# Kernel optimization log

Hardware: AMD Instinct MI355X
Metric: run time of the kernel (lower is better)

Reference implementation:

```python
import jax, jax.numpy as jnp
import numpy as np

N = 40000    # nodes
E = 400000   # edges
H = 128      # hidden_channels
G = 50       # num_gaussians
L = 3        # num_interactions
NG = 256     # number of graphs in the batch
CUTOFF = 6.0


def setup_inputs() -> dict:
    key = jax.random.key(0)
    ks = jax.random.split(key, 16)

    def w(k, shape, fan_in):
        return (jax.random.normal(k, shape, jnp.float32) / np.float32(np.sqrt(fan_in)))

    inp = {}
    inp["atomic_numbers"] = jax.random.randint(ks[0], (N,), 0, 100)
    inp["pos"] = jax.random.normal(ks[1], (N, 3), jnp.float32) * 5.0
    inp["edge_index"] = jax.random.randint(ks[2], (2, E), 0, N)
    inp["batch_ids"] = jnp.sort(jax.random.randint(ks[3], (N,), 0, NG))
    inp["embed"] = w(ks[4], (100, H), 1.0)
    inp["msg_w1"] = w(ks[5], (L, H, H), H)
    inp["msg_b1"] = jnp.zeros((L, H), jnp.float32)
    inp["msg_w2"] = w(ks[6], (L, H, 3 * H), H)
    inp["msg_b2"] = jnp.zeros((L, 3 * H), jnp.float32)
    inp["filt_w"] = w(ks[7], (L, G, 3 * H), G)
    inp["filt_b"] = jnp.zeros((L, 3 * H), jnp.float32)
    inp["vec_w"] = w(ks[8], (L, H, 2 * H), H)
    inp["upd_w1"] = w(ks[9], (L, 2 * H, H), 2 * H)
    inp["upd_b1"] = jnp.zeros((L, H), jnp.float32)
    inp["upd_w2"] = w(ks[10], (L, H, 3 * H), H)
    inp["upd_b2"] = jnp.zeros((L, 3 * H), jnp.float32)
    inp["ro_w1"] = w(ks[11], (H, H // 2), H)
    inp["ro_b1"] = jnp.zeros((H // 2,), jnp.float32)
    inp["ro_w2"] = w(ks[12], (H // 2, 1), H // 2)
    inp["ro_b2"] = jnp.zeros((1,), jnp.float32)
    return inp


def _painn(atomic_numbers, pos, edge_index, batch_ids, embed,
           msg_w1, msg_b1, msg_w2, msg_b2, filt_w, filt_b, vec_w,
           upd_w1, upd_b1, upd_w2, upd_b2, ro_w1, ro_b1, ro_w2, ro_b2):
    src, dst = edge_index[0], edge_index[1]
    n = atomic_numbers.shape[0]

    # geometry
    dvec = pos[src] - pos[dst]                              # [E,3]
    dist = jnp.linalg.norm(dvec, axis=-1)                   # [E]
    dvec_n = dvec / (dist[:, None] + 1e-8)                  # [E,3]

    # Gaussian smearing (RBF expansion of distances)
    offset = jnp.linspace(0.0, CUTOFF, G).astype(jnp.float32)
    coeff = -0.5 / (offset[1] - offset[0]) ** 2
    rbf = jnp.exp(coeff * (dist[:, None] - offset[None, :]) ** 2)  # [E,G]

    s = embed[atomic_numbers]                               # [N,H]
    v = jnp.zeros((n, 3, H), s.dtype)                       # [N,3,H]

    for i in range(L):
        # --- message block ---
        w = rbf @ filt_w[i] + filt_b[i]                     # [E,3H]
        s_all = jax.nn.relu(s @ msg_w1[i] + msg_b1[i]) @ msg_w2[i] + msg_b2[i]  # [N,3H]
        gate = s_all[src] * w                               # [E,3H]
        g0, g1, g2 = jnp.split(gate, 3, axis=-1)            # each [E,H]
        ds_e = g0
        dv_e = v[src] * g1[:, None, :] + dvec_n[:, :, None] * g2[:, None, :]  # [E,3,H]
        ds = jax.ops.segment_sum(ds_e, dst, num_segments=n)
        dv = jax.ops.segment_sum(dv_e, dst, num_segments=n)
        s = s + ds
        v = v + dv

        # --- update block ---
        vt = v @ vec_w[i]                                   # [N,3,2H]
        V1, V2 = jnp.split(vt, 2, axis=-1)                  # [N,3,H] each
        v_norm = jnp.linalg.norm(V1, axis=1)                # [N,H]
        u = (jax.nn.relu(jnp.concatenate([s, v_norm], axis=-1) @ upd_w1[i] + upd_b1[i])
             @ upd_w2[i] + upd_b2[i])                       # [N,3H]
        a, b, c = jnp.split(u, 3, axis=-1)
        s = s + a
        v = v * b[:, None, :] + V2 * c[:, None, :]

    # readout + global mean pool
    y = jax.nn.relu(s @ ro_w1 + ro_b1) @ ro_w2 + ro_b2      # [N,1]
    summed = jax.ops.segment_sum(y, batch_ids, num_segments=NG)
    counts = jax.ops.segment_sum(jnp.ones((n, 1), y.dtype), batch_ids, num_segments=NG)
    return summed / jnp.maximum(counts, 1.0)                # [NG,1]


def reference(atomic_numbers, pos, edge_index, batch_ids, embed,
              msg_w1, msg_b1, msg_w2, msg_b2, filt_w, filt_b, vec_w,
              upd_w1, upd_b1, upd_w2, upd_b2, ro_w1, ro_b1, ro_w2, ro_b2):
    return _painn(atomic_numbers, pos, edge_index, batch_ids, embed,
                  msg_w1, msg_b1, msg_w2, msg_b2, filt_w, filt_b, vec_w,
                  upd_w1, upd_b1, upd_w2, upd_b2, ro_w1, ro_b1, ro_w2, ro_b2)
```

## Files before the change

kernel.cpp:

```cpp
#include <hip/hip_runtime.h>
#include <hip/hip_bf16.h>
#include <math.h>


#define N_NODES 40000
#define N_EDGES 400000
#define NGAUSS  50
#define NLAY    3
#define NGRAPH  256

#define WS_BYTES (448ull * 1024 * 1024)
__device__ __align__(256) unsigned char g_ws[WS_BYTES];

typedef __attribute__((ext_vector_type(8))) short short8;
typedef __attribute__((ext_vector_type(4))) float f32x4;

__device__ __forceinline__ float relu_f(float x) { return fmaxf(x, 0.f); }
__device__ __forceinline__ unsigned short f2b(float x) {
  __hip_bfloat16 h = __float2bfloat16(x);
  return *reinterpret_cast<unsigned short*>(&h);
}
__device__ __forceinline__ float b2f(unsigned short u) {
  return __uint_as_float(((unsigned int)u) << 16);
}
__device__ __forceinline__ float b2f_lo(unsigned int u) {
  return __uint_as_float(u << 16);
}
__device__ __forceinline__ float b2f_hi(unsigned int u) {
  return __uint_as_float(u & 0xffff0000u);
}

__global__ __launch_bounds__(256) void cvt_kernel(const float* __restrict__ in,
                                                  unsigned short* __restrict__ out,
                                                  int n) {
  int i = blockIdx.x * 256 + threadIdx.x;
  if (i < n) out[i] = f2b(in[i]);
}

__global__ __launch_bounds__(256) void geom_kernel(const int* __restrict__ src,
                                                   const int* __restrict__ dst,
                                                   const float* __restrict__ pos,
                                                   float4* __restrict__ geom) {
  int e = blockIdx.x * 256 + threadIdx.x;
  if (e >= N_EDGES) return;
  int s = src[e], d = dst[e];
  float dx = pos[s * 3 + 0] - pos[d * 3 + 0];
  float dy = pos[s * 3 + 1] - pos[d * 3 + 1];
  float dz = pos[s * 3 + 2] - pos[d * 3 + 2];
  float dist = sqrtf(dx * dx + dy * dy + dz * dz);
  float inv = 1.f / (dist + 1e-8f);
  geom[e] = make_float4(dx * inv, dy * inv, dz * inv, dist);
}

__global__ __launch_bounds__(256) void hist_kernel(const int* __restrict__ dst,
                                                   int* __restrict__ deg) {
  int e = blockIdx.x * 256 + threadIdx.x;
  if (e < N_EDGES) atomicAdd(&deg[dst[e]], 1);
}

__global__ __launch_bounds__(1024) void scan_kernel(const int* __restrict__ deg,
                                                    int* __restrict__ off, int n) {
  __shared__ int wsum[16];
  __shared__ int ctot;
  int t = threadIdx.x, lane = t & 63, w = t >> 6;
  int carry = 0;
  for (int base = 0; base < n; base += 1024) {
    int i = base + t;
    int v = (i < n) ? deg[i] : 0;
    int x = v;
#pragma unroll
    for (int dd = 1; dd < 64; dd <<= 1) {
      int y = __shfl_up(x, dd);
      if (lane >= dd) x += y;
    }
    if (lane == 63) wsum[w] = x;
    __syncthreads();
    if (w == 0 && lane < 16) {
      int self = wsum[lane];
      int xs = self;
#pragma unroll
      for (int dd = 1; dd < 16; dd <<= 1) {
        int y = __shfl_up(xs, dd);
        if (lane >= dd) xs += y;
      }
      wsum[lane] = xs - self;
      if (lane == 15) ctot = xs;
    }
    __syncthreads();
    if (i < n) off[i] = carry + wsum[w] + (x - v);
    carry += ctot;
    __syncthreads();
  }
  if (t == 0) off[n] = carry;
}

__global__ __launch_bounds__(256) void fill_kernel(const int* __restrict__ dst,
                                                   const int* __restrict__ off,
                                                   int* __restrict__ cursor,
                                                   int* __restrict__ eid) {
  int e = blockIdx.x * 256 + threadIdx.x;
  if (e >= N_EDGES) return;
  int d = dst[e];
  int p = atomicAdd(&cursor[d], 1);
  eid[off[d] + p] = e;
}

__global__ __launch_bounds__(256) void init_kernel(const int* __restrict__ z,
                                                   const float* __restrict__ embed,
                                                   float* __restrict__ s,
                                                   unsigned short* __restrict__ sb,
                                                   unsigned short* __restrict__ vb) {
  int idx = blockIdx.x * 256 + threadIdx.x;
  if (idx < N_NODES * 384) vb[idx] = 0;
  if (idx < N_NODES * 128) {
    int node = idx >> 7, c = idx & 127;
    float val = embed[z[node] * 128 + c];
    s[idx] = val;
    sb[idx] = f2b(val);
  }
}

#define KMAX 256
__global__ __launch_bounds__(256) void gemm_bf16(
    const unsigned short* __restrict__ A1, int lda1,
    const unsigned short* __restrict__ A2, int lda2, int kSplit,
    const unsigned short* __restrict__ B, int ldb,
    const float* __restrict__ bias,
    void* __restrict__ C, int ldc, int M, int K, int doRelu, int outBf16) {
  __shared__ unsigned int Bt32[64][KMAX / 2 + 4];
  int t = threadIdx.x;
  int lane = t & 63, w = t >> 6;
  int n0 = blockIdx.x * 64, m0 = blockIdx.y * 128;
  {
    int c4 = (t & 15) * 4;
    for (int k = (t >> 4) * 2; k < K; k += 32) {
      uint2 va = *(const uint2*)&B[(size_t)k * ldb + n0 + c4];
      uint2 vb = *(const uint2*)&B[(size_t)(k + 1) * ldb + n0 + c4];
      Bt32[c4 + 0][k >> 1] = (va.x & 0xffffu) | (vb.x << 16);
      Bt32[c4 + 1][k >> 1] = (va.x >> 16) | (vb.x & 0xffff0000u);
      Bt32[c4 + 2][k >> 1] = (va.y & 0xffffu) | (vb.y << 16);
      Bt32[c4 + 3][k >> 1] = (va.y >> 16) | (vb.y & 0xffff0000u);
    }
  }
  __syncthreads();

  int row = lane & 15;
  int kg = lane >> 4;

  f32x4 acc[2][4];
#pragma unroll
  for (int rf = 0; rf < 2; ++rf)
#pragma unroll
    for (int nf = 0; nf < 4; ++nf) acc[rf][nf] = (f32x4){0.f, 0.f, 0.f, 0.f};

  for (int ks = 0; ks < K; ks += 32) {
    int kk = ks + kg * 8;
    short8 af[2];
#pragma unroll
    for (int rf = 0; rf < 2; ++rf) {
      int mrow = m0 + w * 32 + rf * 16 + row;
      if (mrow >= M) mrow = M - 1;
      const unsigned short* Ap;
      int kloc;
      if (kk < kSplit) { Ap = A1 + (size_t)mrow * lda1; kloc = kk; }
      else             { Ap = A2 + (size_t)mrow * lda2; kloc = kk - kSplit; }
      af[rf] = *(const short8*)&Ap[kloc];
    }
#pragma unroll
    for (int nf = 0; nf < 4; ++nf) {
      short8 bf = *(const short8*)((const unsigned short*)Bt32[nf * 16 + row] + kk);
#pragma unroll
      for (int rf = 0; rf < 2; ++rf)
        acc[rf][nf] = __builtin_amdgcn_mfma_f32_16x16x32_bf16(af[rf], bf,
                                                              acc[rf][nf], 0, 0, 0);
    }
  }

#pragma unroll
  for (int rf = 0; rf < 2; ++rf)
#pragma unroll
    for (int nf = 0; nf < 4; ++nf)
#pragma unroll
      for (int r = 0; r < 4; ++r) {
        int gr = m0 + w * 32 + rf * 16 + kg * 4 + r;
        int gc = n0 + nf * 16 + row;
        if (gr < M) {
          float val = acc[rf][nf][r] + (bias ? bias[gc] : 0.f);
          if (doRelu) val = relu_f(val);
          if (outBf16) ((unsigned short*)C)[(size_t)gr * ldc + gc] = f2b(val);
          else         ((float*)C)[(size_t)gr * ldc + gc] = val;
        }
      }
}

__global__ __launch_bounds__(256) void msg_kernel(const int* __restrict__ off,
                                                  const int* __restrict__ eid_arr,
                                                  const int* __restrict__ src_arr,
                                                  const float4* __restrict__ geom,
                                                  const unsigned short* __restrict__ s_all_b,
                                                  const unsigned short* __restrict__ fwb,
                                                  const float* __restrict__ fb,
                                                  const float* __restrict__ s_in,
                                                  const unsigned short* __restrict__ v_in_b,
                                                  float* __restrict__ s_out,
                                                  unsigned short* __restrict__ s_out_b,
                                                  unsigned short* __restrict__ v_out_b) {
  int node = blockIdx.x * 4 + (threadIdx.x >> 6);
  if (node >= N_NODES) return;
  int lane = threadIdx.x & 63;
  int c2 = lane * 2;
  const float DELTA = 6.0f / 49.0f;
  const float INVD = 49.0f / 6.0f;
  const float CO = -0.5f * INVD * INVD;
  float fbr[3][2];
#pragma unroll
  for (int jj = 0; jj < 3; ++jj) {
    float2 f = *(const float2*)&fb[jj * 128 + c2];
    fbr[jj][0] = f.x; fbr[jj][1] = f.y;
  }
  float ds[2] = {0.f, 0.f};
  float dv[3][2] = {{0.f}};
  int e0 = off[node], e1 = off[node + 1];

  for (int q = e0; q < e1; ++q) {
    int e = eid_arr[q];
    int s = src_arr[e];
    float4 gm = geom[e];
    float d = gm.w;
    float wv[3][2];
#pragma unroll
    for (int jj = 0; jj < 3; ++jj) { wv[jj][0] = fbr[jj][0]; wv[jj][1] = fbr[jj][1]; }
    int glo = max(0, (int)ceilf(d * INVD - 8.f));
    int ghi = min(NGAUSS - 1, (int)floorf(d * INVD + 8.f));
    for (int g = glo; g <= ghi; ++g) {
      float diff = d - g * DELTA;
      float r = __expf(CO * diff * diff);
      const unsigned short* fr = fwb + (size_t)g * 384 + c2;
#pragma unroll
      for (int jj = 0; jj < 3; ++jj) {
        unsigned int f = *(const unsigned int*)&fr[jj * 128];
        wv[jj][0] = fmaf(r, b2f_lo(f), wv[jj][0]);
        wv[jj][1] = fmaf(r, b2f_hi(f), wv[jj][1]);
      }
    }
    const unsigned short* pas = s_all_b + (size_t)s * 384 + c2;
    const unsigned short* pav = v_in_b + (size_t)s * 384 + c2;
    unsigned int a_s[3] = {*(const unsigned int*)&pas[0],
                           *(const unsigned int*)&pas[128],
                           *(const unsigned int*)&pas[256]};
    unsigned int a_v[3] = {*(const unsigned int*)&pav[0],
                           *(const unsigned int*)&pav[128],
                           *(const unsigned int*)&pav[256]};
    float gt[3][2];
#pragma unroll
    for (int jj = 0; jj < 3; ++jj) {
      gt[jj][0] = b2f_lo(a_s[jj]) * wv[jj][0];
      gt[jj][1] = b2f_hi(a_s[jj]) * wv[jj][1];
    }
    ds[0] += gt[0][0];
    ds[1] += gt[0][1];
    float dn[3] = {gm.x, gm.y, gm.z};
#pragma unroll
    for (int dd = 0; dd < 3; ++dd) {
      dv[dd][0] = fmaf(b2f_lo(a_v[dd]), gt[1][0], fmaf(dn[dd], gt[2][0], dv[dd][0]));
      dv[dd][1] = fmaf(b2f_hi(a_v[dd]), gt[1][1], fmaf(dn[dd], gt[2][1], dv[dd][1]));
    }
  }

  size_t sb = (size_t)node * 128 + c2;
  float2 si = *(const float2*)&s_in[sb];
  float2 so = make_float2(si.x + ds[0], si.y + ds[1]);
  *(float2*)&s_out[sb] = so;
  *(unsigned int*)&s_out_b[sb] =
      (unsigned int)f2b(so.x) | ((unsigned int)f2b(so.y) << 16);
#pragma unroll
  for (int dd = 0; dd < 3; ++dd) {
    size_t vb = (size_t)node * 384 + dd * 128 + c2;
    unsigned int vi = *(const unsigned int*)&v_in_b[vb];
    float vo0 = b2f_lo(vi) + dv[dd][0];
    float vo1 = b2f_hi(vi) + dv[dd][1];
    *(unsigned int*)&v_out_b[vb] =
        (unsigned int)f2b(vo0) | ((unsigned int)f2b(vo1) << 16);
  }
}

__global__ __launch_bounds__(256) void vnorm_kernel(const unsigned short* __restrict__ V12b,
                                                    unsigned short* __restrict__ vnb) {
  int idx = blockIdx.x * 256 + threadIdx.x;
  if (idx >= N_NODES * 32) return;
  int node = idx >> 5, c4 = (idx & 31) * 4;
  size_t b = (size_t)node * 768 + c4;
  ushort4 x = *(const ushort4*)&V12b[b];
  ushort4 y = *(const ushort4*)&V12b[b + 256];
  ushort4 zz = *(const ushort4*)&V12b[b + 512];
  ushort4 o;
  o.x = f2b(sqrtf(b2f(x.x) * b2f(x.x) + b2f(y.x) * b2f(y.x) + b2f(zz.x) * b2f(zz.x)));
  o.y = f2b(sqrtf(b2f(x.y) * b2f(x.y) + b2f(y.y) * b2f(y.y) + b2f(zz.y) * b2f(zz.y)));
  o.z = f2b(sqrtf(b2f(x.z) * b2f(x.z) + b2f(y.z) * b2f(y.z) + b2f(zz.z) * b2f(zz.z)));
  o.w = f2b(sqrtf(b2f(x.w) * b2f(x.w) + b2f(y.w) * b2f(y.w) + b2f(zz.w) * b2f(zz.w)));
  *(ushort4*)&vnb[(size_t)node * 128 + c4] = o;
}

__global__ __launch_bounds__(256) void update_kernel(const float* __restrict__ s_msg,
                                                     const unsigned short* __restrict__ v_msg_b,
                                                     const unsigned short* __restrict__ u_b,
                                                     const unsigned short* __restrict__ V12b,
                                                     float* __restrict__ s_out,
                                                     unsigned short* __restrict__ s_out_b,
                                                     unsigned short* __restrict__ v_out_b) {
  int idx = blockIdx.x * 256 + threadIdx.x;
  if (idx >= N_NODES * 32) return;
  int node = idx >> 5, c4 = (idx & 31) * 4;
  size_t ub = (size_t)node * 384 + c4;
  ushort4 a4 = *(const ushort4*)&u_b[ub];
  ushort4 b4 = *(const ushort4*)&u_b[ub + 128];
  ushort4 c4v = *(const ushort4*)&u_b[ub + 256];
  size_t sb = (size_t)node * 128 + c4;
  float4 sm = *(const float4*)&s_msg[sb];
  float4 so = make_float4(sm.x + b2f(a4.x), sm.y + b2f(a4.y),
                          sm.z + b2f(a4.z), sm.w + b2f(a4.w));
  *(float4*)&s_out[sb] = so;
  ushort4 sob = {f2b(so.x), f2b(so.y), f2b(so.z), f2b(so.w)};
  *(ushort4*)&s_out_b[sb] = sob;
  float bb[4] = {b2f(b4.x), b2f(b4.y), b2f(b4.z), b2f(b4.w)};
  float cc[4] = {b2f(c4v.x), b2f(c4v.y), b2f(c4v.z), b2f(c4v.w)};
#pragma unroll
  for (int dd = 0; dd < 3; ++dd) {
    size_t vb = (size_t)node * 384 + dd * 128 + c4;
    size_t vbv = (size_t)node * 768 + dd * 256 + 128 + c4;
    ushort4 vm = *(const ushort4*)&v_msg_b[vb];
    ushort4 v2 = *(const ushort4*)&V12b[vbv];
    ushort4 vo;
    vo.x = f2b(b2f(vm.x) * bb[0] + b2f(v2.x) * cc[0]);
    vo.y = f2b(b2f(vm.y) * bb[1] + b2f(v2.y) * cc[1]);
    vo.z = f2b(b2f(vm.z) * bb[2] + b2f(v2.z) * cc[2]);
    vo.w = f2b(b2f(vm.w) * bb[3] + b2f(v2.w) * cc[3]);
    *(ushort4*)&v_out_b[vb] = vo;
  }
}

__global__ __launch_bounds__(256) void readout2_kernel(const float* __restrict__ ro_h,
                                                       const float* __restrict__ w2,
                                                       const int* __restrict__ batch,
                                                       float* __restrict__ pool,
                                                       float* __restrict__ cnt) {
  int node = blockIdx.x * 4 + (threadIdx.x >> 6);
  if (node >= N_NODES) return;
  int lane = threadIdx.x & 63;
  float y = ro_h[(size_t)node * 64 + lane] * w2[lane];
#pragma unroll
  for (int o = 32; o > 0; o >>= 1) y += __shfl_xor(y, o);
  if (lane == 0) {
    int b = batch[node];
    atomicAdd(&pool[b], y);
    atomicAdd(&cnt[b], 1.0f);
  }
}

__global__ void final_kernel(const float* __restrict__ pool,
                             const float* __restrict__ cnt,
                             const float* __restrict__ b2,
                             float* __restrict__ out) {
  int g = threadIdx.x;
  if (g < NGRAPH) out[g] = (pool[g] + cnt[g] * b2[0]) / fmaxf(cnt[g], 1.0f);
}

extern "C" void kernel_launch(void* const* d_in, const int* in_sizes, int n_in,
                              void* d_out, int out_size, void* d_ws, size_t ws_size,
                              hipStream_t stream) {
  const int*   z      = (const int*)d_in[0];
  const float* pos    = (const float*)d_in[1];
  const int*   esrc   = (const int*)d_in[2];
  const int*   edst   = esrc + N_EDGES;
  const int*   batch  = (const int*)d_in[3];
  const float* embed  = (const float*)d_in[4];
  const float* msg_w1 = (const float*)d_in[5];
  const float* msg_b1 = (const float*)d_in[6];
  const float* msg_w2 = (const float*)d_in[7];
  const float* msg_b2 = (const float*)d_in[8];
  const float* filt_w = (const float*)d_in[9];
  const float* filt_b = (const float*)d_in[10];
  const float* vec_w  = (const float*)d_in[11];
  const float* upd_w1 = (const float*)d_in[12];
  const float* upd_b1 = (const float*)d_in[13];
  const float* upd_w2 = (const float*)d_in[14];
  const float* upd_b2 = (const float*)d_in[15];
  const float* ro_w1  = (const float*)d_in[16];
  const float* ro_b1  = (const float*)d_in[17];
  const float* ro_w2  = (const float*)d_in[18];
  const float* ro_b2  = (const float*)d_in[19];
  (void)in_sizes; (void)n_in; (void)out_size;

  void* wsp = nullptr;
  if (hipGetSymbolAddress(&wsp, HIP_SYMBOL(g_ws)) != hipSuccess || wsp == nullptr) {
    wsp = d_ws;
  }
  char* wsb = (char*)wsp;
  size_t o = 0;
  auto alloc = [&](size_t bytes) -> void* {
    void* p = wsb + o;
    o += (bytes + 255) & ~(size_t)255;
    return p;
  };
  float4* geom   = (float4*)alloc(sizeof(float4) * N_EDGES);
  int* csr_off   = (int*)alloc(4ull * (N_NODES + 1));
  int* deg       = (int*)alloc(4ull * N_NODES);
  int* cursor    = (int*)alloc(4ull * N_NODES);
  int* csr_eid   = (int*)alloc(4ull * N_EDGES);
  float* sA      = (float*)alloc(4ull * N_NODES * 128);
  float* sB      = (float*)alloc(4ull * N_NODES * 128);
  float* ro_h    = (float*)alloc(4ull * N_NODES * 64);
  unsigned short* s_all_b = (unsigned short*)alloc(2ull * N_NODES * 384);
  unsigned short* sAb    = (unsigned short*)alloc(2ull * N_NODES * 128);
  unsigned short* sBb    = (unsigned short*)alloc(2ull * N_NODES * 128);
  unsigned short* vAb    = (unsigned short*)alloc(2ull * N_NODES * 384);
  unsigned short* vBb    = (unsigned short*)alloc(2ull * N_NODES * 384);
  unsigned short* vnb    = (unsigned short*)alloc(2ull * N_NODES * 128);
  unsigned short* hidden = (unsigned short*)alloc(2ull * N_NODES * 128);
  unsigned short* Vbuf_b = (unsigned short*)alloc(2ull * N_NODES * 768);
  unsigned short* ubuf_b = (unsigned short*)alloc(2ull * N_NODES * 384);
  unsigned short* wb_m1  = (unsigned short*)alloc(2ull * NLAY * 128 * 128);
  unsigned short* wb_m2  = (unsigned short*)alloc(2ull * NLAY * 128 * 384);
  unsigned short* wb_vw  = (unsigned short*)alloc(2ull * NLAY * 128 * 256);
  unsigned short* wb_u1  = (unsigned short*)alloc(2ull * NLAY * 256 * 128);
  unsigned short* wb_u2  = (unsigned short*)alloc(2ull * NLAY * 128 * 384);
  unsigned short* wb_fw  = (unsigned short*)alloc(2ull * NLAY * 50 * 384);
  unsigned short* wb_ro  = (unsigned short*)alloc(2ull * 128 * 64);
  float* pool    = (float*)alloc(4ull * NGRAPH);
  float* cnt     = (float*)alloc(4ull * NGRAPH);

  if (wsb == (char*)d_ws && o > ws_size) return;

  hipMemsetAsync(deg, 0, 4ull * N_NODES, stream);
  hipMemsetAsync(cursor, 0, 4ull * N_NODES, stream);
  hipMemsetAsync(pool, 0, 4ull * NGRAPH, stream);
  hipMemsetAsync(cnt, 0, 4ull * NGRAPH, stream);

  auto cvt = [&](const float* in, unsigned short* out, int n) {
    cvt_kernel<<<(n + 255) / 256, 256, 0, stream>>>(in, out, n);
  };
  cvt(msg_w1, wb_m1, NLAY * 128 * 128);
  cvt(msg_w2, wb_m2, NLAY * 128 * 384);
  cvt(vec_w,  wb_vw, NLAY * 128 * 256);
  cvt(upd_w1, wb_u1, NLAY * 256 * 128);
  cvt(upd_w2, wb_u2, NLAY * 128 * 384);
  cvt(filt_w, wb_fw, NLAY * 50 * 384);
  cvt(ro_w1,  wb_ro, 128 * 64);

  geom_kernel<<<(N_EDGES + 255) / 256, 256, 0, stream>>>(esrc, edst, pos, geom);
  hist_kernel<<<(N_EDGES + 255) / 256, 256, 0, stream>>>(edst, deg);
  scan_kernel<<<1, 1024, 0, stream>>>(deg, csr_off, N_NODES);
  fill_kernel<<<(N_EDGES + 255) / 256, 256, 0, stream>>>(edst, csr_off, cursor, csr_eid);
  init_kernel<<<(N_NODES * 384 + 255) / 256, 256, 0, stream>>>(z, embed, sA, sAb, vAb);

  const int BIG = 1 << 30;
  const int GY40 = (N_NODES + 127) / 128;
  const int GY120 = (N_NODES * 3 + 127) / 128;
  for (int i = 0; i < NLAY; ++i) {
    const float* mb1 = msg_b1 + (size_t)i * 128;
    const float* mb2 = msg_b2 + (size_t)i * 384;
    const float* fbv = filt_b + (size_t)i * 384;
    const float* ub1 = upd_b1 + (size_t)i * 128;
    const float* ub2 = upd_b2 + (size_t)i * 384;
    const unsigned short* m1 = wb_m1 + (size_t)i * 128 * 128;
    const unsigned short* m2 = wb_m2 + (size_t)i * 128 * 384;
    const unsigned short* vw = wb_vw + (size_t)i * 128 * 256;
    const unsigned short* u1 = wb_u1 + (size_t)i * 256 * 128;
    const unsigned short* u2 = wb_u2 + (size_t)i * 128 * 384;
    const unsigned short* fwb = wb_fw + (size_t)i * 50 * 384;

    gemm_bf16<<<dim3(2, GY40), 256, 0, stream>>>(sAb, 128, sAb, 128, BIG, m1, 128, mb1,
                                                 hidden, 128, N_NODES, 128, 1, 1);
    gemm_bf16<<<dim3(6, GY40), 256, 0, stream>>>(hidden, 128, hidden, 128, BIG, m2, 384,
                                                 mb2, s_all_b, 384, N_NODES, 128, 0, 1);
    msg_kernel<<<N_NODES / 4, 256, 0, stream>>>(csr_off, csr_eid, esrc, geom,
                                                s_all_b, fwb, fbv, sA, vAb,
                                                sB, sBb, vBb);
    gemm_bf16<<<dim3(4, GY120), 256, 0, stream>>>(vBb, 128, vBb, 128, BIG, vw, 256,
                                                  nullptr, Vbuf_b, 256, N_NODES * 3,
                                                  128, 0, 1);
    vnorm_kernel<<<(N_NODES * 32 + 255) / 256, 256, 0, stream>>>(Vbuf_b, vnb);
    gemm_bf16<<<dim3(2, GY40), 256, 0, stream>>>(sBb, 128, vnb, 128, 128, u1, 128, ub1,
                                                 hidden, 128, N_NODES, 256, 1, 1);
    gemm_bf16<<<dim3(6, GY40), 256, 0, stream>>>(hidden, 128, hidden, 128, BIG, u2, 384,
                                                 ub2, ubuf_b, 384, N_NODES, 128, 0, 1);
    update_kernel<<<(N_NODES * 32 + 255) / 256, 256, 0, stream>>>(sB, vBb, ubuf_b,
                                                                  Vbuf_b, sA, sAb, vAb);
  }

  gemm_bf16<<<dim3(1, GY40), 256, 0, stream>>>(sAb, 128, sAb, 128, BIG, wb_ro, 64,
                                               ro_b1, ro_h, 64, N_NODES, 128, 1, 0);
  readout2_kernel<<<N_NODES / 4, 256, 0, stream>>>(ro_h, ro_w2, batch, pool, cnt);
  final_kernel<<<1, 256, 0, stream>>>(pool, cnt, ro_b2, (float*)d_out);
}
```

Measured before the change: 1.253 ms.

## Keep A tile in registers and loop over all N columns per block

Result: slower. 1.443 ms (+15.2%).

```diff
diff --git a/kernel.cpp b/kernel.cpp
--- a/kernel.cpp
+++ b/kernel.cpp
@@ -120,77 +120,88 @@
   }
 }
 
-#define KMAX 256
+template <int K>
 __global__ __launch_bounds__(256) void gemm_bf16(
     const unsigned short* __restrict__ A1, int lda1,
     const unsigned short* __restrict__ A2, int lda2, int kSplit,
     const unsigned short* __restrict__ B, int ldb,
     const float* __restrict__ bias,
-    void* __restrict__ C, int ldc, int M, int K, int doRelu, int outBf16) {
-  __shared__ unsigned int Bt32[64][KMAX / 2 + 4];
+    void* __restrict__ C, int ldc, int M, int N, int doRelu, int outBf16) {
+  constexpr int KS = K / 32;
+  __shared__ unsigned int Bt32[64][K / 2 + 4];
   int t = threadIdx.x;
   int lane = t & 63, w = t >> 6;
-  int n0 = blockIdx.x * 64, m0 = blockIdx.y * 128;
-  {
-    int c4 = (t & 15) * 4;
-    for (int k = (t >> 4) * 2; k < K; k += 32) {
-      uint2 va = *(const uint2*)&B[(size_t)k * ldb + n0 + c4];
-      uint2 vb = *(const uint2*)&B[(size_t)(k + 1) * ldb + n0 + c4];
-      Bt32[c4 + 0][k >> 1] = (va.x & 0xffffu) | (vb.x << 16);
-      Bt32[c4 + 1][k >> 1] = (va.x >> 16) | (vb.x & 0xffff0000u);
-      Bt32[c4 + 2][k >> 1] = (va.y & 0xffffu) | (vb.y << 16);
-      Bt32[c4 + 3][k >> 1] = (va.y >> 16) | (vb.y & 0xffff0000u);
-    }
-  }
-  __syncthreads();
-
+  int m0 = blockIdx.x * 128;
   int row = lane & 15;
   int kg = lane >> 4;
 
-  f32x4 acc[2][4];
-#pragma unroll
-  for (int rf = 0; rf < 2; ++rf)
-#pragma unroll
-    for (int nf = 0; nf < 4; ++nf) acc[rf][nf] = (f32x4){0.f, 0.f, 0.f, 0.f};
-
-  for (int ks = 0; ks < K; ks += 32) {
-    int kk = ks + kg * 8;
-    short8 af[2];
-#pragma unroll
-    for (int rf = 0; rf < 2; ++rf) {
-      int mrow = m0 + w * 32 + rf * 16 + row;
-      if (mrow >= M) mrow = M - 1;
+  short8 af[2][KS];
+#pragma unroll
+  for (int rf = 0; rf < 2; ++rf) {
+    int mrow = m0 + w * 32 + rf * 16 + row;
+    if (mrow >= M) mrow = M - 1;
+#pragma unroll
+    for (int ks = 0; ks < KS; ++ks) {
+      int kk = ks * 32 + kg * 8;
       const unsigned short* Ap;
       int kloc;
       if (kk < kSplit) { Ap = A1 + (size_t)mrow * lda1; kloc = kk; }
       else             { Ap = A2 + (size_t)mrow * lda2; kloc = kk - kSplit; }
-      af[rf] = *(const short8*)&Ap[kloc];
-    }
-#pragma unroll
-    for (int nf = 0; nf < 4; ++nf) {
-      short8 bf = *(const short8*)((const unsigned short*)Bt32[nf * 16 + row] + kk);
-#pragma unroll
-      for (int rf = 0; rf < 2; ++rf)
-        acc[rf][nf] = __builtin_amdgcn_mfma_f32_16x16x32_bf16(af[rf], bf,
-                                                              acc[rf][nf], 0, 0, 0);
-    }
-  }
-
-#pragma unroll
-  for (int rf = 0; rf < 2; ++rf)
-#pragma unroll
-    for (int nf = 0; nf < 4; ++nf)
-#pragma unroll
-      for (int r = 0; r < 4; ++r) {
-        int gr = m0 + w * 32 + rf * 16 + kg * 4 + r;
-        int gc = n0 + nf * 16 + row;
-        if (gr < M) {
-          float val = acc[rf][nf][r] + (bias ? bias[gc] : 0.f);
-          if (doRelu) val = relu_f(val);
-          if (outBf16) ((unsigned short*)C)[(size_t)gr * ldc + gc] = f2b(val);
-          else         ((float*)C)[(size_t)gr * ldc + gc] = val;
+      af[rf][ks] = *(const short8*)&Ap[kloc];
+    }
+  }
+
+  for (int n0 = 0; n0 < N; n0 += 64) {
+    {
+      int c4 = (t & 15) * 4;
+#pragma unroll
+      for (int k = (t >> 4) * 2; k < K; k += 32) {
+        uint2 va = *(const uint2*)&B[(size_t)k * ldb + n0 + c4];
+        uint2 vb = *(const uint2*)&B[(size_t)(k + 1) * ldb + n0 + c4];
+        Bt32[c4 + 0][k >> 1] = (va.x & 0xffffu) | (vb.x << 16);
+        Bt32[c4 + 1][k >> 1] = (va.x >> 16) | (vb.x & 0xffff0000u);
+        Bt32[c4 + 2][k >> 1] = (va.y & 0xffffu) | (vb.y << 16);
+        Bt32[c4 + 3][k >> 1] = (va.y >> 16) | (vb.y & 0xffff0000u);
+      }
+    }
+    __syncthreads();
+
+    f32x4 acc[2][4];
+#pragma unroll
+    for (int rf = 0; rf < 2; ++rf)
+#pragma unroll
+      for (int nf = 0; nf < 4; ++nf) acc[rf][nf] = (f32x4){0.f, 0.f, 0.f, 0.f};
+
+#pragma unroll
+    for (int ks = 0; ks < KS; ++ks) {
+      int kk = ks * 32 + kg * 8;
+#pragma unroll
+      for (int nf = 0; nf < 4; ++nf) {
+        short8 bf = *(const short8*)((const unsigned short*)Bt32[nf * 16 + row] + kk);
+#pragma unroll
+        for (int rf = 0; rf < 2; ++rf)
+          acc[rf][nf] = __builtin_amdgcn_mfma_f32_16x16x32_bf16(af[rf][ks], bf,
+                                                                acc[rf][nf], 0, 0, 0);
+      }
+    }
+
+#pragma unroll
+    for (int rf = 0; rf < 2; ++rf)
+#pragma unroll
+      for (int nf = 0; nf < 4; ++nf)
+#pragma unroll
+        for (int r = 0; r < 4; ++r) {
+          int gr = m0 + w * 32 + rf * 16 + kg * 4 + r;
+          int gc = n0 + nf * 16 + row;
+          if (gr < M) {
+            float val = acc[rf][nf][r] + (bias ? bias[gc] : 0.f);
+            if (doRelu) val = relu_f(val);
+            if (outBf16) ((unsigned short*)C)[(size_t)gr * ldc + gc] = f2b(val);
+            else         ((float*)C)[(size_t)gr * ldc + gc] = val;
+          }
         }
-      }
+    __syncthreads();
+  }
 }
 
 __global__ __launch_bounds__(256) void msg_kernel(const int* __restrict__ off,
@@ -469,27 +480,27 @@
     const unsigned short* u2 = wb_u2 + (size_t)i * 128 * 384;
     const unsigned short* fwb = wb_fw + (size_t)i * 50 * 384;
 
-    gemm_bf16<<<dim3(2, GY40), 256, 0, stream>>>(sAb, 128, sAb, 128, BIG, m1, 128, mb1,
-                                                 hidden, 128, N_NODES, 128, 1, 1);
-    gemm_bf16<<<dim3(6, GY40), 256, 0, stream>>>(hidden, 128, hidden, 128, BIG, m2, 384,
-                                                 mb2, s_all_b, 384, N_NODES, 128, 0, 1);
+    gemm_bf16<128><<<GY40, 256, 0, stream>>>(sAb, 128, sAb, 128, BIG, m1, 128, mb1,
+                                             hidden, 128, N_NODES, 128, 1, 1);
+    gemm_bf16<128><<<GY40, 256, 0, stream>>>(hidden, 128, hidden, 128, BIG, m2, 384,
+                                             mb2, s_all_b, 384, N_NODES, 384, 0, 1);
     msg_kernel<<<N_NODES / 4, 256, 0, stream>>>(csr_off, csr_eid, esrc, geom,
                                                 s_all_b, fwb, fbv, sA, vAb,
                                                 sB, sBb, vBb);
-    gemm_bf16<<<dim3(4, GY120), 256, 0, stream>>>(vBb, 128, vBb, 128, BIG, vw, 256,
-                                                  nullptr, Vbuf_b, 256, N_NODES * 3,
-                                                  128, 0, 1);
+    gemm_bf16<128><<<GY120, 256, 0, stream>>>(vBb, 128, vBb, 128, BIG, vw, 256,
+                                              nullptr, Vbuf_b, 256, N_NODES * 3, 256,
+                                              0, 1);
     vnorm_kernel<<<(N_NODES * 32 + 255) / 256, 256, 0, stream>>>(Vbuf_b, vnb);
-    gemm_bf16<<<dim3(2, GY40), 256, 0, stream>>>(sBb, 128, vnb, 128, 128, u1, 128, ub1,
-                                                 hidden, 128, N_NODES, 256, 1, 1);
-    gemm_bf16<<<dim3(6, GY40), 256, 0, stream>>>(hidden, 128, hidden, 128, BIG, u2, 384,
-                                                 ub2, ubuf_b, 384, N_NODES, 128, 0, 1);
+    gemm_bf16<256><<<GY40, 256, 0, stream>>>(sBb, 128, vnb, 128, 128, u1, 128, ub1,
+                                             hidden, 128, N_NODES, 128, 1, 1);
+    gemm_bf16<128><<<GY40, 256, 0, stream>>>(hidden, 128, hidden, 128, BIG, u2, 384,
+                                             ub2, ubuf_b, 384, N_NODES, 384, 0, 1);
     update_kernel<<<(N_NODES * 32 + 255) / 256, 256, 0, stream>>>(sB, vBb, ubuf_b,
                                                                   Vbuf_b, sA, sAb, vAb);
   }
 
-  gemm_bf16<<<dim3(1, GY40), 256, 0, stream>>>(sAb, 128, sAb, 128, BIG, wb_ro, 64,
-                                               ro_b1, ro_h, 64, N_NODES, 128, 1, 0);
+  gemm_bf16<128><<<GY40, 256, 0, stream>>>(sAb, 128, sAb, 128, BIG, wb_ro, 64, ro_b1,
+                                           ro_h, 64, N_NODES, 64, 1, 0);
   readout2_kernel<<<N_NODES / 4, 256, 0, stream>>>(ro_h, ro_w2, batch, pool, cnt);
   final_kernel<<<1, 256, 0, stream>>>(pool, cnt, ro_b2, (float*)d_out);
 }
```

## Interleave message/vector/filter layouts and pre-sort edge data into CSR order

Applied to the files above, without the earlier changes.

New measurement: 1.264 ms. Within noise of the previous version (+0.8%).

```diff
diff --git a/kernel.cpp b/kernel.cpp
--- a/kernel.cpp
+++ b/kernel.cpp
@@ -29,12 +29,27 @@
 __device__ __forceinline__ float b2f_hi(unsigned int u) {
   return __uint_as_float(u & 0xffff0000u);
 }
+__device__ __forceinline__ unsigned int pk(float a, float b) {
+  return (unsigned int)f2b(a) | ((unsigned int)f2b(b) << 16);
+}
 
 __global__ __launch_bounds__(256) void cvt_kernel(const float* __restrict__ in,
                                                   unsigned short* __restrict__ out,
                                                   int n) {
   int i = blockIdx.x * 256 + threadIdx.x;
   if (i < n) out[i] = f2b(in[i]);
+}
+
+__global__ __launch_bounds__(256) void cvt_fw_kernel(const float* __restrict__ in,
+                                                     unsigned short* __restrict__ out) {
+  int idx = blockIdx.x * 256 + threadIdx.x;
+  if (idx >= NLAY * NGAUSS * 384) return;
+  int l = idx / (NGAUSS * 384);
+  int rem = idx % (NGAUSS * 384);
+  int g = rem / 384, c = rem % 384;
+  int j = c >> 7, cc = c & 127;
+  out[(size_t)l * NGAUSS * 384 + g * 384 + (cc >> 1) * 6 + j * 2 + (cc & 1)] =
+      f2b(in[idx]);
 }
 
 __global__ __launch_bounds__(256) void geom_kernel(const int* __restrict__ src,
@@ -94,24 +109,29 @@
   if (t == 0) off[n] = carry;
 }
 
-__global__ __launch_bounds__(256) void fill_kernel(const int* __restrict__ dst,
+__global__ __launch_bounds__(256) void fill_kernel(const int* __restrict__ src,
+                                                   const int* __restrict__ dst,
                                                    const int* __restrict__ off,
                                                    int* __restrict__ cursor,
-                                                   int* __restrict__ eid) {
+                                                   const float4* __restrict__ geom,
+                                                   int* __restrict__ srcs,
+                                                   float4* __restrict__ geoms) {
   int e = blockIdx.x * 256 + threadIdx.x;
   if (e >= N_EDGES) return;
   int d = dst[e];
   int p = atomicAdd(&cursor[d], 1);
-  eid[off[d] + p] = e;
+  int pos = off[d] + p;
+  srcs[pos] = src[e];
+  geoms[pos] = geom[e];
 }
 
 __global__ __launch_bounds__(256) void init_kernel(const int* __restrict__ z,
                                                    const float* __restrict__ embed,
                                                    float* __restrict__ s,
                                                    unsigned short* __restrict__ sb,
-                                                   unsigned short* __restrict__ vb) {
+                                                   unsigned short* __restrict__ vax) {
   int idx = blockIdx.x * 256 + threadIdx.x;
-  if (idx < N_NODES * 384) vb[idx] = 0;
+  if (idx < N_NODES * 384) vax[idx] = 0;
   if (idx < N_NODES * 128) {
     int node = idx >> 7, c = idx & 127;
     float val = embed[z[node] * 128 + c];
@@ -126,7 +146,7 @@
     const unsigned short* __restrict__ A2, int lda2, int kSplit,
     const unsigned short* __restrict__ B, int ldb,
     const float* __restrict__ bias,
-    void* __restrict__ C, int ldc, int M, int K, int doRelu, int outBf16) {
+    void* __restrict__ C, int ldc, int M, int K, int doRelu, int outMode) {
   __shared__ unsigned int Bt32[64][KMAX / 2 + 4];
   int t = threadIdx.x;
   int lane = t & 63, w = t >> 6;
@@ -187,21 +207,27 @@
         if (gr < M) {
           float val = acc[rf][nf][r] + (bias ? bias[gc] : 0.f);
           if (doRelu) val = relu_f(val);
-          if (outBf16) ((unsigned short*)C)[(size_t)gr * ldc + gc] = f2b(val);
-          else         ((float*)C)[(size_t)gr * ldc + gc] = val;
+          if (outMode == 0) {
+            ((float*)C)[(size_t)gr * ldc + gc] = val;
+          } else if (outMode == 1) {
+            ((unsigned short*)C)[(size_t)gr * ldc + gc] = f2b(val);
+          } else {
+            int j = gc >> 7, cc = gc & 127;
+            ((unsigned short*)C)[(size_t)gr * 384 + (cc >> 1) * 6 + j * 2 + (cc & 1)]
+                = f2b(val);
+          }
         }
       }
 }
 
 __global__ __launch_bounds__(256) void msg_kernel(const int* __restrict__ off,
-                                                  const int* __restrict__ eid_arr,
-                                                  const int* __restrict__ src_arr,
-                                                  const float4* __restrict__ geom,
-                                                  const unsigned short* __restrict__ s_all_b,
-                                                  const unsigned short* __restrict__ fwb,
+                                                  const int* __restrict__ srcs,
+                                                  const float4* __restrict__ geoms,
+                                                  const unsigned int* __restrict__ s_allX,
+                                                  const unsigned int* __restrict__ fwX,
                                                   const float* __restrict__ fb,
                                                   const float* __restrict__ s_in,
-                                                  const unsigned short* __restrict__ v_in_b,
+                                                  const unsigned int* __restrict__ vAx,
                                                   float* __restrict__ s_out,
                                                   unsigned short* __restrict__ s_out_b,
                                                   unsigned short* __restrict__ v_out_b) {
@@ -223,9 +249,8 @@
   int e0 = off[node], e1 = off[node + 1];
 
   for (int q = e0; q < e1; ++q) {
-    int e = eid_arr[q];
-    int s = src_arr[e];
-    float4 gm = geom[e];
+    int s = srcs[q];
+    float4 gm = geoms[q];
     float d = gm.w;
     float wv[3][2];
 #pragma unroll
@@ -235,35 +260,34 @@
     for (int g = glo; g <= ghi; ++g) {
       float diff = d - g * DELTA;
       float r = __expf(CO * diff * diff);
-      const unsigned short* fr = fwb + (size_t)g * 384 + c2;
-#pragma unroll
-      for (int jj = 0; jj < 3; ++jj) {
-        unsigned int f = *(const unsigned int*)&fr[jj * 128];
-        wv[jj][0] = fmaf(r, b2f_lo(f), wv[jj][0]);
-        wv[jj][1] = fmaf(r, b2f_hi(f), wv[jj][1]);
-      }
-    }
-    const unsigned short* pas = s_all_b + (size_t)s * 384 + c2;
-    const unsigned short* pav = v_in_b + (size_t)s * 384 + c2;
-    unsigned int a_s[3] = {*(const unsigned int*)&pas[0],
-                           *(const unsigned int*)&pas[128],
-                           *(const unsigned int*)&pas[256]};
-    unsigned int a_v[3] = {*(const unsigned int*)&pav[0],
-                           *(const unsigned int*)&pav[128],
-                           *(const unsigned int*)&pav[256]};
+      const unsigned int* fr = fwX + g * 192 + lane * 3;
+      unsigned int f0 = fr[0], f1 = fr[1], f2v = fr[2];
+      wv[0][0] = fmaf(r, b2f_lo(f0), wv[0][0]);
+      wv[0][1] = fmaf(r, b2f_hi(f0), wv[0][1]);
+      wv[1][0] = fmaf(r, b2f_lo(f1), wv[1][0]);
+      wv[1][1] = fmaf(r, b2f_hi(f1), wv[1][1]);
+      wv[2][0] = fmaf(r, b2f_lo(f2v), wv[2][0]);
+      wv[2][1] = fmaf(r, b2f_hi(f2v), wv[2][1]);
+    }
+    const unsigned int* ps = s_allX + (size_t)s * 192 + lane * 3;
+    const unsigned int* pv = vAx + (size_t)s * 192 + lane * 3;
+    unsigned int s0 = ps[0], s1 = ps[1], s2 = ps[2];
+    unsigned int v0 = pv[0], v1 = pv[1], v2 = pv[2];
     float gt[3][2];
-#pragma unroll
-    for (int jj = 0; jj < 3; ++jj) {
-      gt[jj][0] = b2f_lo(a_s[jj]) * wv[jj][0];
-      gt[jj][1] = b2f_hi(a_s[jj]) * wv[jj][1];
-    }
+    gt[0][0] = b2f_lo(s0) * wv[0][0];
+    gt[0][1] = b2f_hi(s0) * wv[0][1];
+    gt[1][0] = b2f_lo(s1) * wv[1][0];
+    gt[1][1] = b2f_hi(s1) * wv[1][1];
+    gt[2][0] = b2f_lo(s2) * wv[2][0];
+    gt[2][1] = b2f_hi(s2) * wv[2][1];
     ds[0] += gt[0][0];
     ds[1] += gt[0][1];
     float dn[3] = {gm.x, gm.y, gm.z};
+    unsigned int vvs[3] = {v0, v1, v2};
 #pragma unroll
     for (int dd = 0; dd < 3; ++dd) {
-      dv[dd][0] = fmaf(b2f_lo(a_v[dd]), gt[1][0], fmaf(dn[dd], gt[2][0], dv[dd][0]));
-      dv[dd][1] = fmaf(b2f_hi(a_v[dd]), gt[1][1], fmaf(dn[dd], gt[2][1], dv[dd][1]));
+      dv[dd][0] = fmaf(b2f_lo(vvs[dd]), gt[1][0], fmaf(dn[dd], gt[2][0], dv[dd][0]));
+      dv[dd][1] = fmaf(b2f_hi(vvs[dd]), gt[1][1], fmaf(dn[dd], gt[2][1], dv[dd][1]));
     }
   }
 
@@ -271,16 +295,16 @@
   float2 si = *(const float2*)&s_in[sb];
   float2 so = make_float2(si.x + ds[0], si.y + ds[1]);
   *(float2*)&s_out[sb] = so;
-  *(unsigned int*)&s_out_b[sb] =
-      (unsigned int)f2b(so.x) | ((unsigned int)f2b(so.y) << 16);
+  *(unsigned int*)&s_out_b[sb] = pk(so.x, so.y);
+  const unsigned int* pv0 = vAx + (size_t)node * 192 + lane * 3;
+  unsigned int vi0 = pv0[0], vi1 = pv0[1], vi2 = pv0[2];
+  unsigned int vis[3] = {vi0, vi1, vi2};
 #pragma unroll
   for (int dd = 0; dd < 3; ++dd) {
     size_t vb = (size_t)node * 384 + dd * 128 + c2;
-    unsigned int vi = *(const unsigned int*)&v_in_b[vb];
-    float vo0 = b2f_lo(vi) + dv[dd][0];
-    float vo1 = b2f_hi(vi) + dv[dd][1];
-    *(unsigned int*)&v_out_b[vb] =
-        (unsigned int)f2b(vo0) | ((unsigned int)f2b(vo1) << 16);
+    float vo0 = b2f_lo(vis[dd]) + dv[dd][0];
+    float vo1 = b2f_hi(vis[dd]) + dv[dd][1];
+    *(unsigned int*)&v_out_b[vb] = pk(vo0, vo1);
   }
 }
 
@@ -307,7 +331,7 @@
                                                      const unsigned short* __restrict__ V12b,
                                                      float* __restrict__ s_out,
                                                      unsigned short* __restrict__ s_out_b,
-                                                     unsigned short* __restrict__ v_out_b) {
+                                                     unsigned int* __restrict__ vAx) {
   int idx = blockIdx.x * 256 + threadIdx.x;
   if (idx >= N_NODES * 32) return;
   int node = idx >> 5, c4 = (idx & 31) * 4;
@@ -324,18 +348,19 @@
   *(ushort4*)&s_out_b[sb] = sob;
   float bb[4] = {b2f(b4.x), b2f(b4.y), b2f(b4.z), b2f(b4.w)};
   float cc[4] = {b2f(c4v.x), b2f(c4v.y), b2f(c4v.z), b2f(c4v.w)};
+  int l0 = c4 >> 1;
 #pragma unroll
   for (int dd = 0; dd < 3; ++dd) {
     size_t vb = (size_t)node * 384 + dd * 128 + c4;
     size_t vbv = (size_t)node * 768 + dd * 256 + 128 + c4;
     ushort4 vm = *(const ushort4*)&v_msg_b[vb];
     ushort4 v2 = *(const ushort4*)&V12b[vbv];
-    ushort4 vo;
-    vo.x = f2b(b2f(vm.x) * bb[0] + b2f(v2.x) * cc[0]);
-    vo.y = f2b(b2f(vm.y) * bb[1] + b2f(v2.y) * cc[1]);
-    vo.z = f2b(b2f(vm.z) * bb[2] + b2f(v2.z) * cc[2]);
-    vo.w = f2b(b2f(vm.w) * bb[3] + b2f(v2.w) * cc[3]);
-    *(ushort4*)&v_out_b[vb] = vo;
+    float o0 = b2f(vm.x) * bb[0] + b2f(v2.x) * cc[0];
+    float o1 = b2f(vm.y) * bb[1] + b2f(v2.y) * cc[1];
+    float o2 = b2f(vm.z) * bb[2] + b2f(v2.z) * cc[2];
+    float o3 = b2f(vm.w) * bb[3] + b2f(v2.w) * cc[3];
+    vAx[(size_t)node * 192 + l0 * 3 + dd] = pk(o0, o1);
+    vAx[(size_t)node * 192 + (l0 + 1) * 3 + dd] = pk(o2, o3);
   }
 }
 
@@ -403,17 +428,18 @@
     return p;
   };
   float4* geom   = (float4*)alloc(sizeof(float4) * N_EDGES);
+  float4* geoms  = (float4*)alloc(sizeof(float4) * N_EDGES);
+  int* srcs      = (int*)alloc(4ull * N_EDGES);
   int* csr_off   = (int*)alloc(4ull * (N_NODES + 1));
   int* deg       = (int*)alloc(4ull * N_NODES);
   int* cursor    = (int*)alloc(4ull * N_NODES);
-  int* csr_eid   = (int*)alloc(4ull * N_EDGES);
   float* sA      = (float*)alloc(4ull * N_NODES * 128);
   float* sB      = (float*)alloc(4ull * N_NODES * 128);
   float* ro_h    = (float*)alloc(4ull * N_NODES * 64);
-  unsigned short* s_all_b = (unsigned short*)alloc(2ull * N_NODES * 384);
+  unsigned short* s_allX = (unsigned short*)alloc(2ull * N_NODES * 384);
   unsigned short* sAb    = (unsigned short*)alloc(2ull * N_NODES * 128);
   unsigned short* sBb    = (unsigned short*)alloc(2ull * N_NODES * 128);
-  unsigned short* vAb    = (unsigned short*)alloc(2ull * N_NODES * 384);
+  unsigned short* vAx    = (unsigned short*)alloc(2ull * N_NODES * 384);
   unsigned short* vBb    = (unsigned short*)alloc(2ull * N_NODES * 384);
   unsigned short* vnb    = (unsigned short*)alloc(2ull * N_NODES * 128);
   unsigned short* hidden = (unsigned short*)alloc(2ull * N_NODES * 128);
@@ -424,7 +450,7 @@
   unsigned short* wb_vw  = (unsigned short*)alloc(2ull * NLAY * 128 * 256);
   unsigned short* wb_u1  = (unsigned short*)alloc(2ull * NLAY * 256 * 128);
   unsigned short* wb_u2  = (unsigned short*)alloc(2ull * NLAY * 128 * 384);
-  unsigned short* wb_fw  = (unsigned short*)alloc(2ull * NLAY * 50 * 384);
+  unsigned short* wb_fwX = (unsigned short*)alloc(2ull * NLAY * 50 * 384);
   unsigned short* wb_ro  = (unsigned short*)alloc(2ull * 128 * 64);
   float* pool    = (float*)alloc(4ull * NGRAPH);
   float* cnt     = (float*)alloc(4ull * NGRAPH);
@@ -444,14 +470,15 @@
   cvt(vec_w,  wb_vw, NLAY * 128 * 256);
   cvt(upd_w1, wb_u1, NLAY * 256 * 128);
   cvt(upd_w2, wb_u2, NLAY * 128 * 384);
-  cvt(filt_w, wb_fw, NLAY * 50 * 384);
   cvt(ro_w1,  wb_ro, 128 * 64);
+  cvt_fw_kernel<<<(NLAY * NGAUSS * 384 + 255) / 256, 256, 0, stream>>>(filt_w, wb_fwX);
 
   geom_kernel<<<(N_EDGES + 255) / 256, 256, 0, stream>>>(esrc, edst, pos, geom);
   hist_kernel<<<(N_EDGES + 255) / 256, 256, 0, stream>>>(edst, deg);
   scan_kernel<<<1, 1024, 0, stream>>>(deg, csr_off, N_NODES);
-  fill_kernel<<<(N_EDGES + 255) / 256, 256, 0, stream>>>(edst, csr_off, cursor, csr_eid);
-  init_kernel<<<(N_NODES * 384 + 255) / 256, 256, 0, stream>>>(z, embed, sA, sAb, vAb);
+  fill_kernel<<<(N_EDGES + 255) / 256, 256, 0, stream>>>(esrc, edst, csr_off, cursor,
+                                                         geom, srcs, geoms);
+  init_kernel<<<(N_NODES * 384 + 255) / 256, 256, 0, stream>>>(z, embed, sA, sAb, vAx);
 
   const int BIG = 1 << 30;
   const int GY40 = (N_NODES + 127) / 128;
@@ -467,14 +494,15 @@
     const unsigned short* vw = wb_vw + (size_t)i * 128 * 256;
     const unsigned short* u1 = wb_u1 + (size_t)i * 256 * 128;
     const unsigned short* u2 = wb_u2 + (size_t)i * 128 * 384;
-    const unsigned short* fwb = wb_fw + (size_t)i * 50 * 384;
+    const unsigned int* fwX = (const unsigned int*)(wb_fwX + (size_t)i * 50 * 384);
 
     gemm_bf16<<<dim3(2, GY40), 256, 0, stream>>>(sAb, 128, sAb, 128, BIG, m1, 128, mb1,
                                                  hidden, 128, N_NODES, 128, 1, 1);
     gemm_bf16<<<dim3(6, GY40), 256, 0, stream>>>(hidden, 128, hidden, 128, BIG, m2, 384,
-                                                 mb2, s_all_b, 384, N_NODES, 128, 0, 1);
-    msg_kernel<<<N_NODES / 4, 256, 0, stream>>>(csr_off, csr_eid, esrc, geom,
-                                                s_all_b, fwb, fbv, sA, vAb,
+                                                 mb2, s_allX, 384, N_NODES, 128, 0, 2);
+    msg_kernel<<<N_NODES / 4, 256, 0, stream>>>(csr_off, srcs, geoms,
+                                                (const unsigned int*)s_allX, fwX, fbv,
+                                                sA, (const unsigned int*)vAx,
                                                 sB, sBb, vBb);
     gemm_bf16<<<dim3(4, GY120), 256, 0, stream>>>(vBb, 128, vBb, 128, BIG, vw, 256,
                                                   nullptr, Vbuf_b, 256, N_NODES * 3,
@@ -485,7 +513,8 @@
     gemm_bf16<<<dim3(6, GY40), 256, 0, stream>>>(hidden, 128, hidden, 128, BIG, u2, 384,
                                                  ub2, ubuf_b, 384, N_NODES, 128, 0, 1);
     update_kernel<<<(N_NODES * 32 + 255) / 256, 256, 0, stream>>>(sB, vBb, ubuf_b,
-                                                                  Vbuf_b, sA, sAb, vAb);
+                                                                  Vbuf_b, sA, sAb,
+                                                                  (unsigned int*)vAx);
   }
 
   gemm_bf16<<<dim3(1, GY40), 256, 0, stream>>>(sAb, 128, sAb, 128, BIG, wb_ro, 64,
```
